# Kernel tuning notes

Hardware: AMD Instinct MI355X
Metric: run time of the kernel (lower is better)

Reference implementation:

```python
import jax, jax.numpy as jnp
import numpy as np

B, CIN, H, W = 256, 1280, 7, 7
A, NCLS, HID, NGT = 9, 20, 128, 40
OUT_DIM = 5 * A + NCLS  # 65


def setup_inputs() -> dict:
    key = jax.random.key(0)
    ks = jax.random.split(key, 8)
    features = jax.random.normal(ks[0], (B, CIN, H, W), jnp.float32)
    # grid: (x, y) centers of each feature cell, in feature-map coordinates
    grid = jax.random.uniform(ks[1], (B, H, W, 2), jnp.float32) * 7.0
    # GT boxes (x1, y1, x2, y2, class), padded count NGT per image
    xy1 = jax.random.uniform(ks[2], (B, NGT, 2), jnp.float32) * 5.0
    wh = jax.random.uniform(ks[3], (B, NGT, 2), jnp.float32) * 2.0 + 0.5
    cls = jax.random.randint(ks[4], (B, NGT, 1), 0, NCLS).astype(jnp.float32)
    bboxes = jnp.concatenate([xy1, xy1 + wh, cls], axis=-1)
    # anchor shapes (w, h) as in SingleStageDetector.__init__
    anc = jnp.array([[1.0, 1], [2, 2], [3, 3], [4, 4], [5, 5],
                     [2, 3], [3, 2], [3, 5], [5, 3]], jnp.float32)
    W1 = jax.random.normal(ks[5], (HID, CIN), jnp.float32) * 0.02
    b1 = jnp.zeros((HID,), jnp.float32)
    W2 = jax.random.normal(ks[6], (OUT_DIM, HID), jnp.float32) * 0.02
    b2 = jnp.zeros((OUT_DIM,), jnp.float32)
    return dict(features=features, grid=grid, bboxes=bboxes, anc=anc,
                W1=W1, b1=b1, W2=W2, b2=b2)


def reference(features, grid, bboxes, anc, W1, b1, W2, b2):
    Bx = features.shape[0]
    # --- PredictionNetwork (inference mode; dropout is identity at eval) ---
    h = jnp.einsum('bchw,oc->bohw', features, W1) + b1[None, :, None, None]
    h = jax.nn.leaky_relu(h, negative_slope=0.01)
    out = jnp.einsum('bchw,oc->bohw', h, W2) + b2[None, :, None, None]
    conf_scores = jax.nn.sigmoid(out[:, 4 * A:5 * A])          # (B, A, H, W)
    offsets = out[:, :4 * A].reshape(Bx, A, 4, H, W)
    offsets = jnp.concatenate(
        [jax.nn.sigmoid(offsets[:, :, :2]) - 0.5, offsets[:, :, 2:]], axis=2)
    class_scores = out[:, 5 * A:]                               # (B, C, H, W)
    # --- GenerateAnchor: (B, A, H, W, 4) as (x_tl, y_tl, x_br, y_br) ---
    ctr = grid[:, None]                    # (B, 1, H, W, 2)
    half = anc[None, :, None, None, :] / 2  # (1, A, 1, 1, 2)
    anchors = jnp.concatenate([ctr - half, ctr + half], axis=-1)
    # --- IoU: (B, A*H*W, N) ---
    P = anchors.reshape(Bx, -1, 4)          # (B, AHW, 4)
    gt = bboxes[..., :4]                    # (B, N, 4)
    tl = jnp.maximum(P[:, :, None, :2], gt[:, None, :, :2])
    br = jnp.minimum(P[:, :, None, 2:], gt[:, None, :, 2:])
    inter = jnp.prod(jnp.clip(br - tl, 0.0), axis=-1)  # (B, AHW, N)
    # torch code zeroes intersections for proposals with any coord <= 0
    legal = (jnp.min(P, axis=-1) > 0)[..., None]
    inter = inter * legal
    p_area = ((P[:, :, 2] - P[:, :, 0]) * (P[:, :, 3] - P[:, :, 1]))[:, :, None]
    g_area = ((gt[:, :, 2] - gt[:, :, 0]) * (gt[:, :, 3] - gt[:, :, 1]))[:, None, :]
    iou_mat = inter / (g_area + p_area - inter)
    return (conf_scores, offsets, class_scores, iou_mat)
```

## Files before the change

kernel.cpp:

```cpp
#include <hip/hip_runtime.h>


#define CIN_  1280
#define HW_   49
#define HID_  128
#define OUTD_ 65
#define NGT_  40
#define NP_   441

#define CONF_OFF 0
#define OFFS_OFF 112896
#define CLS_OFF  564480
#define IOU_OFF  815360

#define WS_W1F_U32 81920u
#define WS_W2F_U32 5120u

typedef __bf16 bf16x8 __attribute__((ext_vector_type(8)));
typedef float  f32x4  __attribute__((ext_vector_type(4)));

__device__ __forceinline__ unsigned pack2bf(float lo, float hi) {
    unsigned short a = __builtin_bit_cast(unsigned short, (__bf16)lo);
    unsigned short b = __builtin_bit_cast(unsigned short, (__bf16)hi);
    return (unsigned)a | ((unsigned)b << 16);
}
__device__ __forceinline__ float sigmoidf_(float v) { return 1.f / (1.f + __expf(-v)); }

__device__ __forceinline__ bf16x8 ld_frag(const unsigned* p) {
    union { uint4 u; bf16x8 v; } x;
    x.u = *(const uint4*)p;
    return x.v;
}
__device__ __forceinline__ bf16x8 as_bf(uint4 u) {
    union { uint4 u; bf16x8 v; } x; x.u = u; return x.v;
}
__device__ __forceinline__ bf16x8 pack8(const float* v) {
    union { unsigned u[4]; bf16x8 x; } r;
    #pragma unroll
    for (int j = 0; j < 4; ++j) r.u[j] = pack2bf(v[2 * j], v[2 * j + 1]);
    return r.x;
}

__global__ __launch_bounds__(256) void prep_w(
    const float* __restrict__ W1, const float* __restrict__ W2,
    unsigned* __restrict__ ws)
{
    int X = blockIdx.x * 256 + threadIdx.x;
    if (X < (int)WS_W1F_U32) {
        int sub = X & 3, lane = (X >> 2) & 63, f = X >> 8;
        int mt = f & 7, K32 = f >> 3;
        int o = mt * 16 + (lane & 15);
        int c = K32 * 32 + (lane >> 4) * 8 + sub * 2;
        float2 v = *(const float2*)(W1 + o * CIN_ + c);
        ws[X] = pack2bf(v.x, v.y);
    } else {
        int Y = X - (int)WS_W1F_U32;
        int sub = Y & 3, lane = (Y >> 2) & 63, f = Y >> 8;
        int mt2 = f % 5, ks2 = f / 5;
        int o2 = mt2 * 16 + (lane & 15);
        int c = ks2 * 32 + (lane >> 4) * 8 + sub * 2;
        unsigned val = 0;
        if (o2 < OUTD_) {
            float2 v = *(const float2*)(W2 + o2 * HID_ + c);
            val = pack2bf(v.x, v.y);
        }
        ws[WS_W1F_U32 + Y] = val;
    }
}

__global__ __launch_bounds__(256, 4) void fused_main(
    const float* __restrict__ F,
    const float* __restrict__ grd,
    const float* __restrict__ bbox,
    const float* __restrict__ anc,
    const unsigned* __restrict__ wsW,
    const float* __restrict__ B1,
    const float* __restrict__ B2,
    float* __restrict__ out)
{
    __shared__ __align__(16) unsigned smHT[32 * 68];

    const int tid  = threadIdx.x;
    const int id   = blockIdx.x;
    const int half = id >> 8;
    const int b    = id & 255;
    const int lane = tid & 63;
    const int w    = tid >> 6;
    const int quad = lane >> 4;
    const int m16  = lane & 15;
    const int hw0  = half * 32;

    const float* Fb = F + b * (CIN_ * HW_);
    const int colA = hw0 + m16;
    const int colB = min(hw0 + 16 + m16, HW_ - 1);
    const int mt0 = 2 * w, mt1 = 2 * w + 1;
    const uint4* Af = (const uint4*)wsW;

    #define LOADK(k, vA, vB, ra0, ra1)                                       \
        {                                                                    \
            const float* pk = Fb + ((k) * 32 + quad * 8) * 49;               \
            _Pragma("unroll")                                                \
            for (int j = 0; j < 8; ++j) {                                    \
                vA[j] = pk[j * 49 + colA];                                   \
                vB[j] = pk[j * 49 + colB];                                   \
            }                                                                \
            ra0 = Af[((k) * 8 + mt0) * 64 + lane];                           \
            ra1 = Af[((k) * 8 + mt1) * 64 + lane];                           \
        }

    f32x4 acc[2][2] = {{(f32x4)(0.f), (f32x4)(0.f)}, {(f32x4)(0.f), (f32x4)(0.f)}};
    float cA[8], cB[8]; uint4 ca0, ca1;
    LOADK(0, cA, cB, ca0, ca1);
    #pragma unroll
    for (int k = 0; k < 40; ++k) {
        float nA[8], nB[8]; uint4 na0, na1;
        if (k < 39) LOADK(k + 1, nA, nB, na0, na1);
        bf16x8 Bf0 = pack8(cA);
        bf16x8 Bf1 = pack8(cB);
        bf16x8 A0 = as_bf(ca0);
        bf16x8 A1 = as_bf(ca1);
        acc[0][0] = __builtin_amdgcn_mfma_f32_16x16x32_bf16(A0, Bf0, acc[0][0], 0, 0, 0);
        acc[0][1] = __builtin_amdgcn_mfma_f32_16x16x32_bf16(A0, Bf1, acc[0][1], 0, 0, 0);
        acc[1][0] = __builtin_amdgcn_mfma_f32_16x16x32_bf16(A1, Bf0, acc[1][0], 0, 0, 0);
        acc[1][1] = __builtin_amdgcn_mfma_f32_16x16x32_bf16(A1, Bf1, acc[1][1], 0, 0, 0);
        if (k < 39) {
            #pragma unroll
            for (int j = 0; j < 8; ++j) { cA[j] = nA[j]; cB[j] = nB[j]; }
            ca0 = na0; ca1 = na1;
        }
    }

    #pragma unroll
    for (int mo = 0; mo < 2; ++mo) {
        #pragma unroll
        for (int nh = 0; nh < 2; ++nh) {
            int row = nh * 16 + m16;
            #pragma unroll
            for (int rp = 0; rp < 2; ++rp) {
                int o0 = (2 * w + mo) * 16 + quad * 4 + 2 * rp;
                float v0 = acc[mo][nh][2 * rp]     + B1[o0];
                float v1 = acc[mo][nh][2 * rp + 1] + B1[o0 + 1];
                v0 = v0 > 0.f ? v0 : 0.01f * v0;
                v1 = v1 > 0.f ? v1 : 0.01f * v1;
                smHT[row * 68 + (o0 >> 1)] = pack2bf(v0, v1);
            }
        }
    }
    __syncthreads();

    for (int T = w; T < 10; T += 4) {
        int m2 = T % 5, nt2 = T / 5;
        const uint4* A2p = (const uint4*)(wsW + WS_W1F_U32) + m2 * 64 + lane;
        uint4 a20 = A2p[0], a21 = A2p[320], a22 = A2p[640], a23 = A2p[960];
        f32x4 c2 = (f32x4)(0.f);
        const unsigned* Bb = smHT + (nt2 * 16 + m16) * 68 + quad * 4;
        c2 = __builtin_amdgcn_mfma_f32_16x16x32_bf16(as_bf(a20), ld_frag(Bb +  0), c2, 0, 0, 0);
        c2 = __builtin_amdgcn_mfma_f32_16x16x32_bf16(as_bf(a21), ld_frag(Bb + 16), c2, 0, 0, 0);
        c2 = __builtin_amdgcn_mfma_f32_16x16x32_bf16(as_bf(a22), ld_frag(Bb + 32), c2, 0, 0, 0);
        c2 = __builtin_amdgcn_mfma_f32_16x16x32_bf16(as_bf(a23), ld_frag(Bb + 48), c2, 0, 0, 0);
        int hw = hw0 + nt2 * 16 + m16;
        if (hw < HW_) {
            #pragma unroll
            for (int r = 0; r < 4; ++r) {
                int o2 = m2 * 16 + quad * 4 + r;
                if (o2 >= OUTD_) continue;
                float aa = c2[r] + B2[o2];
                unsigned dst; float val;
                if (o2 < 36) {
                    int an9 = o2 >> 2, kk = o2 & 3;
                    val = (kk < 2) ? (sigmoidf_(aa) - 0.5f) : aa;
                    dst = OFFS_OFF + b * 1764 + an9 * 196 + kk * 49 + hw;
                } else if (o2 < 45) {
                    val = sigmoidf_(aa);
                    dst = CONF_OFF + b * 441 + (o2 - 36) * 49 + hw;
                } else {
                    val = aa;
                    dst = CLS_OFF + b * 980 + (o2 - 45) * 49 + hw;
                }
                out[dst] = val;
            }
        }
    }

    {
        int gl = (lane < NGT_) ? lane : 0;
        const float* gb = bbox + b * 200 + gl * 5;
        float gx1 = gb[0], gy1 = gb[1], gx2 = gb[2], gy2 = gb[3];
        float gA = (gx2 - gx1) * (gy2 - gy1);
        const int pstart = half ? 221 : 0;
        const int pend   = half ? NP_ : 221;
        #pragma unroll 4
        for (int p = pstart + w; p < pend; p += 4) {
            int a9 = p / 49, r = p - a9 * 49;
            float2 ct = *(const float2*)(grd + b * 98 + 2 * r);
            float hx = anc[2 * a9] * 0.5f,  hy = anc[2 * a9 + 1] * 0.5f;
            float px1 = ct.x - hx, py1 = ct.y - hy, px2 = ct.x + hx, py2 = ct.y + hy;
            float pA = (px2 - px1) * (py2 - py1);
            float legal = (fminf(fminf(px1, py1), fminf(px2, py2)) > 0.f) ? 1.f : 0.f;
            float tlx = fmaxf(px1, gx1), tly = fmaxf(py1, gy1);
            float brx = fminf(px2, gx2), bry = fminf(py2, gy2);
            float dx = fmaxf(brx - tlx, 0.f), dy = fmaxf(bry - tly, 0.f);
            float inter = dx * dy * legal;
            float iou = __fdividef(inter, gA + pA - inter);
            if (lane < NGT_)
                out[IOU_OFF + b * (NP_ * NGT_) + p * 40 + lane] = iou;
        }
    }
}

extern "C" void kernel_launch(void* const* d_in, const int* in_sizes, int n_in,
                              void* d_out, int out_size, void* d_ws, size_t ws_size,
                              hipStream_t stream) {
    const float* F  = (const float*)d_in[0];
    const float* G  = (const float*)d_in[1];
    const float* BB = (const float*)d_in[2];
    const float* AN = (const float*)d_in[3];
    const float* W1 = (const float*)d_in[4];
    const float* B1 = (const float*)d_in[5];
    const float* W2 = (const float*)d_in[6];
    const float* B2 = (const float*)d_in[7];
    float* out = (float*)d_out;
    unsigned* wsu = (unsigned*)d_ws;

    prep_w<<<340, 256, 0, stream>>>(W1, W2, wsu);
    fused_main<<<512, 256, 0, stream>>>(F, G, BB, AN, wsu, B1, B2, out);
}
```

Baseline: 146.4 us.

## Pre-convert features to bf16 fragment layout and use one 1024-thread block per image

Adds a prep pass that converts the fp32 feature map into bf16 stored in MFMA B-fragment order in workspace. The main kernel then streams coalesced 16-byte fragments with a 3-deep register prefetch instead of strided scalar loads and in-loop packing. Work is regrouped into one 1024-thread block per image with 16 waves, each covering one output tile. This adds an extra write and read of the converted features, in exchange for better load efficiency and latency hiding.

Result: faster. 141.9 us (-3.1%).

```diff
diff --git a/kernel.cpp b/kernel.cpp
--- a/kernel.cpp
+++ b/kernel.cpp
@@ -15,6 +15,7 @@
 
 #define WS_W1F_U32 81920u
 #define WS_W2F_U32 5120u
+#define FB_OFF     87040u
 
 typedef __bf16 bf16x8 __attribute__((ext_vector_type(8)));
 typedef float  f32x4  __attribute__((ext_vector_type(4)));
@@ -34,18 +35,29 @@
 __device__ __forceinline__ bf16x8 as_bf(uint4 u) {
     union { uint4 u; bf16x8 v; } x; x.u = u; return x.v;
 }
-__device__ __forceinline__ bf16x8 pack8(const float* v) {
-    union { unsigned u[4]; bf16x8 x; } r;
-    #pragma unroll
-    for (int j = 0; j < 4; ++j) r.u[j] = pack2bf(v[2 * j], v[2 * j + 1]);
-    return r.x;
-}
-
-__global__ __launch_bounds__(256) void prep_w(
+
+__global__ __launch_bounds__(256) void prep(
+    const float* __restrict__ F,
     const float* __restrict__ W1, const float* __restrict__ W2,
     unsigned* __restrict__ ws)
 {
-    int X = blockIdx.x * 256 + threadIdx.x;
+    if (blockIdx.x < 10240) {
+        int X = blockIdx.x * 256 + threadIdx.x;
+        int lane = X & 63, t = X >> 6;
+        int ct = t & 3, bk = t >> 2;
+        int k32 = bk % 40, b = bk / 40;
+        int quad = lane >> 4, m16 = lane & 15;
+        int col = ct * 16 + m16; if (col > 48) col = 48;
+        const float* p = F + b * (CIN_ * HW_) + (k32 * 32 + quad * 8) * 49 + col;
+        uint4 q;
+        q.x = pack2bf(p[0],   p[49]);
+        q.y = pack2bf(p[98],  p[147]);
+        q.z = pack2bf(p[196], p[245]);
+        q.w = pack2bf(p[294], p[343]);
+        ((uint4*)(ws + FB_OFF))[X] = q;
+        return;
+    }
+    int X = (blockIdx.x - 10240) * 256 + threadIdx.x;
     if (X < (int)WS_W1F_U32) {
         int sub = X & 3, lane = (X >> 2) & 63, f = X >> 8;
         int mt = f & 7, K32 = f >> 3;
@@ -68,8 +80,7 @@
     }
 }
 
-__global__ __launch_bounds__(256, 4) void fused_main(
-    const float* __restrict__ F,
+__global__ __launch_bounds__(1024, 4) void fused_main(
     const float* __restrict__ grd,
     const float* __restrict__ bbox,
     const float* __restrict__ anc,
@@ -78,77 +89,58 @@
     const float* __restrict__ B2,
     float* __restrict__ out)
 {
-    __shared__ __align__(16) unsigned smHT[32 * 68];
+    __shared__ __align__(16) unsigned smHT[64 * 68];
 
     const int tid  = threadIdx.x;
-    const int id   = blockIdx.x;
-    const int half = id >> 8;
-    const int b    = id & 255;
+    const int b    = blockIdx.x;
     const int lane = tid & 63;
     const int w    = tid >> 6;
+    const int wo   = w >> 1;
+    const int ch2  = w & 1;
     const int quad = lane >> 4;
     const int m16  = lane & 15;
-    const int hw0  = half * 32;
-
-    const float* Fb = F + b * (CIN_ * HW_);
-    const int colA = hw0 + m16;
-    const int colB = min(hw0 + 16 + m16, HW_ - 1);
-    const int mt0 = 2 * w, mt1 = 2 * w + 1;
-    const uint4* Af = (const uint4*)wsW;
-
-    #define LOADK(k, vA, vB, ra0, ra1)                                       \
-        {                                                                    \
-            const float* pk = Fb + ((k) * 32 + quad * 8) * 49;               \
-            _Pragma("unroll")                                                \
-            for (int j = 0; j < 8; ++j) {                                    \
-                vA[j] = pk[j * 49 + colA];                                   \
-                vB[j] = pk[j * 49 + colB];                                   \
-            }                                                                \
-            ra0 = Af[((k) * 8 + mt0) * 64 + lane];                           \
-            ra1 = Af[((k) * 8 + mt1) * 64 + lane];                           \
-        }
-
-    f32x4 acc[2][2] = {{(f32x4)(0.f), (f32x4)(0.f)}, {(f32x4)(0.f), (f32x4)(0.f)}};
-    float cA[8], cB[8]; uint4 ca0, ca1;
-    LOADK(0, cA, cB, ca0, ca1);
+
+    const uint4* Ap = (const uint4*)wsW + wo * 64 + lane;
+    const uint4* Fp = (const uint4*)(wsW + FB_OFF) + b * 10240 + ch2 * 128 + lane;
+    #define LD_A(k)    Ap[(k) * 512]
+    #define LD_B(k, j) Fp[(k) * 256 + (j) * 64]
+
+    f32x4 acc[2] = {(f32x4)(0.f), (f32x4)(0.f)};
+    uint4 ar[3], br[3][2];
+    #pragma unroll
+    for (int d = 0; d < 3; ++d) {
+        ar[d] = LD_A(d);
+        br[d][0] = LD_B(d, 0);
+        br[d][1] = LD_B(d, 1);
+    }
     #pragma unroll
     for (int k = 0; k < 40; ++k) {
-        float nA[8], nB[8]; uint4 na0, na1;
-        if (k < 39) LOADK(k + 1, nA, nB, na0, na1);
-        bf16x8 Bf0 = pack8(cA);
-        bf16x8 Bf1 = pack8(cB);
-        bf16x8 A0 = as_bf(ca0);
-        bf16x8 A1 = as_bf(ca1);
-        acc[0][0] = __builtin_amdgcn_mfma_f32_16x16x32_bf16(A0, Bf0, acc[0][0], 0, 0, 0);
-        acc[0][1] = __builtin_amdgcn_mfma_f32_16x16x32_bf16(A0, Bf1, acc[0][1], 0, 0, 0);
-        acc[1][0] = __builtin_amdgcn_mfma_f32_16x16x32_bf16(A1, Bf0, acc[1][0], 0, 0, 0);
-        acc[1][1] = __builtin_amdgcn_mfma_f32_16x16x32_bf16(A1, Bf1, acc[1][1], 0, 0, 0);
-        if (k < 39) {
-            #pragma unroll
-            for (int j = 0; j < 8; ++j) { cA[j] = nA[j]; cB[j] = nB[j]; }
-            ca0 = na0; ca1 = na1;
-        }
+        const int s = k % 3;
+        bf16x8 A = as_bf(ar[s]);
+        acc[0] = __builtin_amdgcn_mfma_f32_16x16x32_bf16(A, as_bf(br[s][0]), acc[0], 0, 0, 0);
+        acc[1] = __builtin_amdgcn_mfma_f32_16x16x32_bf16(A, as_bf(br[s][1]), acc[1], 0, 0, 0);
+        const int kp = (k + 3 < 40) ? k + 3 : 39;
+        ar[s] = LD_A(kp);
+        br[s][0] = LD_B(kp, 0);
+        br[s][1] = LD_B(kp, 1);
     }
 
     #pragma unroll
-    for (int mo = 0; mo < 2; ++mo) {
+    for (int j = 0; j < 2; ++j) {
+        int col = (ch2 * 2 + j) * 16 + m16;
         #pragma unroll
-        for (int nh = 0; nh < 2; ++nh) {
-            int row = nh * 16 + m16;
-            #pragma unroll
-            for (int rp = 0; rp < 2; ++rp) {
-                int o0 = (2 * w + mo) * 16 + quad * 4 + 2 * rp;
-                float v0 = acc[mo][nh][2 * rp]     + B1[o0];
-                float v1 = acc[mo][nh][2 * rp + 1] + B1[o0 + 1];
-                v0 = v0 > 0.f ? v0 : 0.01f * v0;
-                v1 = v1 > 0.f ? v1 : 0.01f * v1;
-                smHT[row * 68 + (o0 >> 1)] = pack2bf(v0, v1);
-            }
+        for (int rp = 0; rp < 2; ++rp) {
+            int o0 = wo * 16 + quad * 4 + 2 * rp;
+            float v0 = acc[j][2 * rp]     + B1[o0];
+            float v1 = acc[j][2 * rp + 1] + B1[o0 + 1];
+            v0 = v0 > 0.f ? v0 : 0.01f * v0;
+            v1 = v1 > 0.f ? v1 : 0.01f * v1;
+            smHT[col * 68 + (o0 >> 1)] = pack2bf(v0, v1);
         }
     }
     __syncthreads();
 
-    for (int T = w; T < 10; T += 4) {
+    for (int T = w; T < 20; T += 16) {
         int m2 = T % 5, nt2 = T / 5;
         const uint4* A2p = (const uint4*)(wsW + WS_W1F_U32) + m2 * 64 + lane;
         uint4 a20 = A2p[0], a21 = A2p[320], a22 = A2p[640], a23 = A2p[960];
@@ -158,7 +150,7 @@
         c2 = __builtin_amdgcn_mfma_f32_16x16x32_bf16(as_bf(a21), ld_frag(Bb + 16), c2, 0, 0, 0);
         c2 = __builtin_amdgcn_mfma_f32_16x16x32_bf16(as_bf(a22), ld_frag(Bb + 32), c2, 0, 0, 0);
         c2 = __builtin_amdgcn_mfma_f32_16x16x32_bf16(as_bf(a23), ld_frag(Bb + 48), c2, 0, 0, 0);
-        int hw = hw0 + nt2 * 16 + m16;
+        int hw = nt2 * 16 + m16;
         if (hw < HW_) {
             #pragma unroll
             for (int r = 0; r < 4; ++r) {
@@ -187,10 +179,8 @@
         const float* gb = bbox + b * 200 + gl * 5;
         float gx1 = gb[0], gy1 = gb[1], gx2 = gb[2], gy2 = gb[3];
         float gA = (gx2 - gx1) * (gy2 - gy1);
-        const int pstart = half ? 221 : 0;
-        const int pend   = half ? NP_ : 221;
         #pragma unroll 4
-        for (int p = pstart + w; p < pend; p += 4) {
+        for (int p = w; p < NP_; p += 16) {
             int a9 = p / 49, r = p - a9 * 49;
             float2 ct = *(const float2*)(grd + b * 98 + 2 * r);
             float hx = anc[2 * a9] * 0.5f,  hy = anc[2 * a9 + 1] * 0.5f;
@@ -222,6 +212,6 @@
     float* out = (float*)d_out;
     unsigned* wsu = (unsigned*)d_ws;
 
-    prep_w<<<340, 256, 0, stream>>>(W1, W2, wsu);
-    fused_main<<<512, 256, 0, stream>>>(F, G, BB, AN, wsu, B1, B2, out);
-}
+    prep<<<10580, 256, 0, stream>>>(F, W1, W2, wsu);
+    fused_main<<<256, 1024, 0, stream>>>(G, BB, AN, wsu, B1, B2, out);
+}
```
